# Optimization experiments

Hardware: AMD Instinct MI355X
Metric: run time of the kernel (lower is better)

Reference implementation:

```python
import jax, jax.numpy as jnp
import numpy as np

EPS = 1e-6
SEARCH_RANGE = 4  # K = 2*R+1 = 9


def setup_inputs() -> dict:
    key = jax.random.key(0)
    k1, k2, k3, k4 = jax.random.split(key, 4)
    B, C, H, W = 4, 128, 128, 240
    E = 64
    F_L = jax.random.normal(k1, (B, C, H, W), dtype=jnp.float32)
    F_R = jax.random.normal(k2, (B, C, H, W), dtype=jnp.float32)
    d0 = jax.random.uniform(k3, (B, 1, H, W), dtype=jnp.float32) * 64.0  # pixel disparity
    phi_w = jax.random.normal(k4, (E, C), dtype=jnp.float32) / np.sqrt(C)  # 1x1 conv weight
    return {"F_L": F_L, "F_R": F_R, "d0": d0, "phi_w": phi_w}


def _embed(x, phi_w):
    # 1x1 conv + channel L2 normalize (cosine embedding)
    y = jnp.einsum('ec,bchw->behw', phi_w, x)
    norm = jnp.sqrt(jnp.sum(y * y, axis=1, keepdims=True)) + EPS
    return y / norm


def reference(F_L, F_R, d0, phi_w):
    R = SEARCH_RANGE
    FL = _embed(F_L, phi_w)  # (B,E,H,W)
    FR = _embed(F_R, phi_w)
    B, E, H, W = FL.shape
    deltas = jnp.arange(-R, R + 1, dtype=FL.dtype)  # (K,)
    xx = jnp.arange(W, dtype=FL.dtype)  # base x grid
    # x' = x - (d0 + delta); align_corners=True grid round-trips to pixel coords exactly,
    # y coordinate is identity, so warp is 1D bilinear along W with border clamp.
    xprime = xx[None, None, None, :] - d0[:, None, 0, :, :] - deltas[None, :, None, None]  # (B,K,H,W)
    x0 = jnp.floor(xprime)
    w = xprime - x0  # bilinear weight
    i0 = jnp.clip(x0.astype(jnp.int32), 0, W - 1)
    i1 = jnp.clip(x0.astype(jnp.int32) + 1, 0, W - 1)
    FR_e = FR[:, None]  # (B,1,E,H,W)
    g0 = jnp.take_along_axis(FR_e, i0[:, :, None, :, :], axis=4)  # (B,K,E,H,W)
    g1 = jnp.take_along_axis(FR_e, i1[:, :, None, :, :], axis=4)
    FR_s = g0 * (1.0 - w)[:, :, None] + g1 * w[:, :, None]
    cost_vol = jnp.einsum('behw,bkehw->bkhw', FL, FR_s)  # (B,K,H,W)
    return cost_vol
```

## Files before the change

kernel.cpp:

```cpp
#include <hip/hip_runtime.h>
#include <hip/hip_bf16.h>

#define NB 4
#define NC 128
#define NH 128
#define NW 240
#define NE 64
#define NK 9
#define PLANE (NH*NW)
#define CHW (NC*PLANE)

typedef __attribute__((ext_vector_type(8))) short short8;
typedef __attribute__((ext_vector_type(4))) float f32x4;
typedef __attribute__((ext_vector_type(2))) __fp16 fp16x2;
typedef __attribute__((ext_vector_type(8))) __fp16 fp16x8;

__device__ __forceinline__ unsigned pkh(float x, float y){
  fp16x2 h = __builtin_amdgcn_cvt_pkrtz(x, y);
  return __builtin_bit_cast(unsigned, h);
}
__device__ __forceinline__ float fdot2u(unsigned a, unsigned b, float c){
#if __has_builtin(__builtin_amdgcn_fdot2)
  return __builtin_amdgcn_fdot2(__builtin_bit_cast(fp16x2,a),
                                __builtin_bit_cast(fp16x2,b), c, false);
#else
  fp16x2 ha = __builtin_bit_cast(fp16x2,a), hb = __builtin_bit_cast(fp16x2,b);
  return c + (float)ha[0]*(float)hb[0] + (float)ha[1]*(float)hb[1];
#endif
}
__device__ __forceinline__ int swz(int r){ return (r ^ (r>>3)) & 7; }

__device__ __forceinline__ void gload_lds16(const float* g, float* lds_u, int lane){
#if __has_builtin(__builtin_amdgcn_global_load_lds)
  __builtin_amdgcn_global_load_lds(
      (const __attribute__((address_space(1))) unsigned*)g,
      (__attribute__((address_space(3))) unsigned*)lds_u, 16, 0, 0);
#else
  *(float4*)(lds_u + 4*lane) = *(const float4*)g;
#endif
}

__global__ __launch_bounds__(1024, 8)
void fused_kernel(const float* __restrict__ xL,
                  const float* __restrict__ xR,
                  const float* __restrict__ d0g,
                  const float* __restrict__ phig,
                  float* __restrict__ outg)
{
  __shared__ __attribute__((aligned(16))) float xs0[7680];
  __shared__ __attribute__((aligned(16))) float xs1[7680];
  __shared__ __attribute__((aligned(16))) unsigned short phis[NE*136];

  const int tid  = threadIdx.x;
  const int lane = tid & 63;
  const int wv   = tid >> 6;
  const int b    = blockIdx.x >> 7;
  const int h    = blockIdx.x & 127;
  const size_t base = (size_t)b*CHW + (size_t)h*NW;
  const int pixbase = (b*NH + h)*NW;

  const int mrow = lane & 15;
  const int kg   = lane >> 4;
  const int nt   = wv;
  const int n    = 16*nt + mrow;

  auto issue_chunk = [&](int q){
    const float* src = (q < 4) ? xL : xR;
    const int cb = 32*(q & 3);
    float* buf = (q & 1) ? xs1 : xs0;
    #pragma unroll
    for (int i = 0; i < 2; ++i) {
      int qq = 2*wv + i;
      if (qq < 30) {
        int g4 = qq*64 + lane;
        int c = g4/60, s4 = g4 - 60*c;
        gload_lds16(src + base + (size_t)(cb + c)*PLANE + 4*s4,
                    buf + qq*256, lane);
      }
    }
  };

  auto gemm_round = [&](const float* bf, int cb, f32x4 (&acc)[4]){
    if (nt < 15) {
      fp16x8 bv;
      #pragma unroll
      for (int j = 0; j < 8; ++j)
        bv[j] = (__fp16)bf[(8*kg + j)*240 + n];
      #pragma unroll
      for (int mt = 0; mt < 4; ++mt) {
        short8 raw = *(const short8*)&phis[(16*mt + mrow)*136 + cb + 8*kg];
        fp16x8 af = __builtin_bit_cast(fp16x8, raw);
        acc[mt] = __builtin_amdgcn_mfma_f32_16x16x32_f16(af, bv, acc[mt], 0, 0, 0);
      }
    }
  };

  auto norm_pack = [&](f32x4 (&acc)[4], uint2 (&pk)[4]){
    float ss = 0.f;
    #pragma unroll
    for (int mt = 0; mt < 4; ++mt)
      #pragma unroll
      for (int r = 0; r < 4; ++r)
        ss += acc[mt][r]*acc[mt][r];
    ss += __shfl_xor(ss, 16, 64);
    ss += __shfl_xor(ss, 32, 64);
    float inv = 1.f/(sqrtf(ss) + 1e-6f);
    #pragma unroll
    for (int mt = 0; mt < 4; ++mt) {
      pk[mt].x = pkh(acc[mt][0]*inv, acc[mt][1]*inv);
      pk[mt].y = pkh(acc[mt][2]*inv, acc[mt][3]*inv);
    }
  };

  auto frag_write = [&](unsigned short* dst, uint2 (&pk)[4]){
    #pragma unroll
    for (int mt = 0; mt < 4; ++mt) {
      int e0 = 16*mt + 4*kg;
      int pos = n*64 + (((e0>>3) ^ swz(n))<<3) + (e0&7);
      *(uint2*)&dst[pos] = pk[mt];
    }
  };

  issue_chunk(0);
  float d0v = (tid < 960) ? d0g[pixbase + (tid >> 2)] : 0.f;
  float4 pr[2];
  #pragma unroll
  for (int i = 0; i < 2; ++i) {
    int idx = i*1024 + tid;
    pr[i] = *(const float4*)(phig + (idx>>5)*128 + 4*(idx&31));
  }
  #pragma unroll
  for (int i = 0; i < 2; ++i) {
    int idx = i*1024 + tid;
    uint2 pk; pk.x = pkh(pr[i].x, pr[i].y); pk.y = pkh(pr[i].z, pr[i].w);
    *(uint2*)&phis[(idx>>5)*136 + 4*(idx&31)] = pk;
  }

  f32x4 accL[4], accR[4];
  #pragma unroll
  for (int mt = 0; mt < 4; ++mt) {
    accL[mt] = (f32x4){0.f,0.f,0.f,0.f};
    accR[mt] = (f32x4){0.f,0.f,0.f,0.f};
  }
  uint2 flpk[4], frpk[4];

  __syncthreads();  issue_chunk(1);  gemm_round(xs0,  0, accL);
  __syncthreads();  issue_chunk(2);  gemm_round(xs1, 32, accL);
  __syncthreads();  issue_chunk(3);  gemm_round(xs0, 64, accL);
  __syncthreads();  issue_chunk(4);  gemm_round(xs1, 96, accL);
  if (nt < 15) norm_pack(accL, flpk);
  __syncthreads();  issue_chunk(5);  gemm_round(xs0,  0, accR);
  __syncthreads();  issue_chunk(6);  gemm_round(xs1, 32, accR);
  __syncthreads();  issue_chunk(7);  gemm_round(xs0, 64, accR);
  __syncthreads();
  unsigned short* FLb = (unsigned short*)xs0;
  if (nt < 15) frag_write(FLb, flpk);
  gemm_round(xs1, 96, accR);
  if (nt < 15) norm_pack(accR, frpk);
  __syncthreads();
  unsigned short* FRb = (unsigned short*)xs1;
  if (nt < 15) frag_write(FRb, frpk);
  __syncthreads();

  float* cvb = (float*)phis;
  if (tid < 960) {
    const int p  = tid >> 2;
    const int eh = tid & 3;
    float xf  = (float)p - d0v;
    float x0  = floorf(xf);
    float wfr = xf - x0;
    int jb = (int)x0 - 4;

    unsigned fl[8];
    #pragma unroll
    for (int i = 0; i < 2; ++i) {
      int c4 = 2*eh + i;
      uint4 raw = *(const uint4*)&FLb[p*64 + ((c4 ^ swz(p))<<3)];
      fl[4*i+0]=raw.x; fl[4*i+1]=raw.y; fl[4*i+2]=raw.z; fl[4*i+3]=raw.w;
    }

    float D[10];
    #pragma unroll
    for (int t = 0; t < 10; ++t) {
      int j = jb + t;
      j = j < 0 ? 0 : (j > NW-1 ? NW-1 : j);
      float s = 0.f;
      #pragma unroll
      for (int i = 0; i < 2; ++i) {
        int c4 = 2*eh + i;
        uint4 raw = *(const uint4*)&FRb[j*64 + ((c4 ^ swz(j))<<3)];
        s = fdot2u(fl[4*i+0], raw.x, s);
        s = fdot2u(fl[4*i+1], raw.y, s);
        s = fdot2u(fl[4*i+2], raw.z, s);
        s = fdot2u(fl[4*i+3], raw.w, s);
      }
      D[t] = s;
    }
    #pragma unroll
    for (int t = 0; t < 10; ++t) {
      D[t] += __shfl_xor(D[t], 1, 64);
      D[t] += __shfl_xor(D[t], 2, 64);
    }

    #define WK(k) { const int t0 = 8-(k); cvb[(k)*NW + p] = (1.f - wfr)*D[t0] + wfr*D[t0+1]; }
    if      (eh == 0) { WK(0) WK(1) WK(2) }
    else if (eh == 1) { WK(3) WK(4) }
    else if (eh == 2) { WK(5) WK(6) }
    else              { WK(7) WK(8) }
    #undef WK
  }
  __syncthreads();

  if (tid < 540) {
    int k = tid/60, w4 = tid - 60*k;
    float4 v = *(const float4*)&cvb[k*NW + 4*w4];
    *(float4*)(outg + (size_t)b*NK*PLANE + (size_t)h*NW + (size_t)k*PLANE + 4*w4) = v;
  }
}

extern "C" void kernel_launch(void* const* d_in, const int* in_sizes, int n_in,
                              void* d_out, int out_size, void* d_ws, size_t ws_size,
                              hipStream_t stream) {
  const float* xL   = (const float*)d_in[0];
  const float* xR   = (const float*)d_in[1];
  const float* d0g  = (const float*)d_in[2];
  const float* phig = (const float*)d_in[3];
  float* outg = (float*)d_out;
  fused_kernel<<<dim3(NB*NH), dim3(1024), 0, stream>>>(xL, xR, d0g, phig, outg);
}
```

Measured before the change: 149.8 us.

## Deepen LDS load pipeline to four buffers with explicit vmcnt waits

Replaces the two-buffer LDS double-buffering with four buffers, keeping three chunk loads in flight. Full __syncthreads are replaced by s_waitcnt vmcnt(N) plus a raw barrier, so only the oldest chunk must land before each MFMA round. The FL and FR fragment writes are merged after the last GEMM, removing one barrier. The cost is LDS use rising to roughly 140KB per block, which likely drops residency from two blocks per CU to one and gives up the overlap between co-resident blocks.

```diff
diff --git a/kernel.cpp b/kernel.cpp
--- a/kernel.cpp
+++ b/kernel.cpp
@@ -40,15 +40,20 @@
 #endif
 }
 
-__global__ __launch_bounds__(1024, 8)
+#define WAITB(N) do {                                                        \
+    asm volatile("s_waitcnt vmcnt(" #N ") lgkmcnt(0)" ::: "memory");         \
+    __builtin_amdgcn_s_barrier();                                            \
+    __builtin_amdgcn_sched_barrier(0);                                       \
+  } while (0)
+
+__global__ __launch_bounds__(1024, 4)
 void fused_kernel(const float* __restrict__ xL,
                   const float* __restrict__ xR,
                   const float* __restrict__ d0g,
                   const float* __restrict__ phig,
                   float* __restrict__ outg)
 {
-  __shared__ __attribute__((aligned(16))) float xs0[7680];
-  __shared__ __attribute__((aligned(16))) float xs1[7680];
+  __shared__ __attribute__((aligned(16))) float bufs[4*7680];
   __shared__ __attribute__((aligned(16))) unsigned short phis[NE*136];
 
   const int tid  = threadIdx.x;
@@ -67,7 +72,7 @@
   auto issue_chunk = [&](int q){
     const float* src = (q < 4) ? xL : xR;
     const int cb = 32*(q & 3);
-    float* buf = (q & 1) ? xs1 : xs0;
+    float* buf = &bufs[(q & 3)*7680];
     #pragma unroll
     for (int i = 0; i < 2; ++i) {
       int qq = 2*wv + i;
@@ -121,7 +126,6 @@
     }
   };
 
-  issue_chunk(0);
   float d0v = (tid < 960) ? d0g[pixbase + (tid >> 2)] : 0.f;
   float4 pr[2];
   #pragma unroll
@@ -129,6 +133,9 @@
     int idx = i*1024 + tid;
     pr[i] = *(const float4*)(phig + (idx>>5)*128 + 4*(idx&31));
   }
+  issue_chunk(0);
+  issue_chunk(1);
+  issue_chunk(2);
   #pragma unroll
   for (int i = 0; i < 2; ++i) {
     int idx = i*1024 + tid;
@@ -144,22 +151,23 @@
   }
   uint2 flpk[4], frpk[4];
 
-  __syncthreads();  issue_chunk(1);  gemm_round(xs0,  0, accL);
-  __syncthreads();  issue_chunk(2);  gemm_round(xs1, 32, accL);
-  __syncthreads();  issue_chunk(3);  gemm_round(xs0, 64, accL);
-  __syncthreads();  issue_chunk(4);  gemm_round(xs1, 96, accL);
+  WAITB(4); issue_chunk(3); gemm_round(&bufs[0*7680],  0, accL);
+  WAITB(4); issue_chunk(4); gemm_round(&bufs[1*7680], 32, accL);
+  WAITB(4); issue_chunk(5); gemm_round(&bufs[2*7680], 64, accL);
+  WAITB(4); issue_chunk(6); gemm_round(&bufs[3*7680], 96, accL);
   if (nt < 15) norm_pack(accL, flpk);
-  __syncthreads();  issue_chunk(5);  gemm_round(xs0,  0, accR);
-  __syncthreads();  issue_chunk(6);  gemm_round(xs1, 32, accR);
-  __syncthreads();  issue_chunk(7);  gemm_round(xs0, 64, accR);
-  __syncthreads();
-  unsigned short* FLb = (unsigned short*)xs0;
-  if (nt < 15) frag_write(FLb, flpk);
-  gemm_round(xs1, 96, accR);
+  WAITB(4); issue_chunk(7); gemm_round(&bufs[0*7680],  0, accR);
+  WAITB(4);                 gemm_round(&bufs[1*7680], 32, accR);
+  WAITB(2);                 gemm_round(&bufs[2*7680], 64, accR);
+  WAITB(0);                 gemm_round(&bufs[3*7680], 96, accR);
   if (nt < 15) norm_pack(accR, frpk);
-  __syncthreads();
-  unsigned short* FRb = (unsigned short*)xs1;
-  if (nt < 15) frag_write(FRb, frpk);
+
+  unsigned short* FLb = (unsigned short*)&bufs[0*7680];
+  unsigned short* FRb = (unsigned short*)&bufs[1*7680];
+  if (nt < 15) {
+    frag_write(FLb, flpk);
+    frag_write(FRb, frpk);
+  }
   __syncthreads();
 
   float* cvb = (float*)phis;
```

After: 153.7 us. 2.6% more time.
